# Optimization experiments

Measured on AMD Instinct MI355X. Metric: run time of the kernel, lower is better.

The kernel has to match this reference:

```python
import jax, jax.numpy as jnp
import numpy as np

B, L, D = 32, 2048, 128
SCALE = 1.0 / float(np.sqrt(D))  # scale = 1/sqrt(dim_K) per docstring


def setup_inputs() -> dict:
    key = jax.random.key(0)
    kq, kk, kv, kb = jax.random.split(key, 4)
    return {
        "Q": jax.random.normal(kq, (B, L, D), dtype=jnp.float32),
        "K": jax.random.normal(kk, (B, L, D), dtype=jnp.float32),
        "V": jax.random.normal(kv, (B, L, D), dtype=jnp.float32),
        "bias": jax.random.normal(kb, (L, L), dtype=jnp.float32),
    }


def reference(Q, K, V, bias):
    # scores = Q @ K^T + bias (bias broadcast over batch), then scale, softmax, @ V
    scores = jnp.einsum("bqd,bkd->bqk", Q, K) + bias[None, :, :]
    attn = jax.nn.softmax(scores * SCALE, axis=-1)  # [B, L, L]
    context = jnp.einsum("bqk,bkd->bqd", attn, V)   # [B, L, D]
    return (context, attn[0])
```

## Files before the change

### kernel.cpp

```cpp
#include <hip/hip_runtime.h>
#include <cstdint>
#include <cstddef>

#define L_ 2048
#define D_ 128
#define B_ 32
#define NT_ 32

static constexpr float SCALE = 0.08838834764831845f;
static constexpr float LOG2E = 1.4426950408889634f;
static constexpr float THR_  = 8.0f;

typedef __bf16 bf16x8 __attribute__((ext_vector_type(8)));
typedef __bf16 bf16x4 __attribute__((ext_vector_type(4)));
typedef float  f32x4  __attribute__((ext_vector_type(4)));
typedef int    i32x4  __attribute__((ext_vector_type(4)));

typedef const __attribute__((address_space(1))) uint32_t* gas_t;
typedef __attribute__((address_space(3))) uint32_t*       las_t;

__device__ __forceinline__ void dma16(const void* g, void* l) {
  __builtin_amdgcn_global_load_lds((gas_t)g, (las_t)l, 16, 0, 0);
}

__device__ __forceinline__ int cperm(int r) {
  return (r & 32) | (((r >> 3) & 1) << 4) | (((r >> 2) & 1) << 3)
       | (((r >> 4) & 1) << 2) | (r & 3);
}

__global__ __launch_bounds__(256) void prep_kv(
    const float* __restrict__ K, const float* __restrict__ V,
    __bf16* __restrict__ gK, __bf16* __restrict__ gVt)
{
  const int b   = blockIdx.x >> 5;
  const int kt  = blockIdx.x & 31;
  const int tid = threadIdx.x;
  const size_t tile = ((size_t)b * NT_ + kt) * 8192;

#pragma unroll
  for (int i = 0; i < 4; ++i) {
    const int g  = tid + i * 256;
    const int r  = g >> 4;
    const int c  = g & 15;
    const int d0 = (c ^ (r & 7)) * 8;
    const float* src = K + ((size_t)b * L_ + kt * 64 + r) * D_ + d0;
    float4 a = *(const float4*)src;
    float4 e = *(const float4*)(src + 4);
    bf16x8 f;
    f[0]=(__bf16)a.x; f[1]=(__bf16)a.y; f[2]=(__bf16)a.z; f[3]=(__bf16)a.w;
    f[4]=(__bf16)e.x; f[5]=(__bf16)e.y; f[6]=(__bf16)e.z; f[7]=(__bf16)e.w;
    *(bf16x8*)((char*)(gK + tile) + r * 256 + c * 16) = f;
  }

  __shared__ alignas(16) __bf16 Vt[8192];
  char* vb = (char*)Vt;
  const int vr     = tid & 63;
  const int vc     = cperm(vr);
  const int vdbase = (tid >> 6) * 32;
  const float* vrow = V + ((size_t)b * L_ + kt * 64 + vr) * D_ + vdbase;
#pragma unroll
  for (int c = 0; c < 8; ++c) {
    float4 v4 = *(const float4*)(vrow + c * 4);
    const int d0 = vdbase + c * 4;
    float vv[4] = {v4.x, v4.y, v4.z, v4.w};
#pragma unroll
    for (int jj = 0; jj < 4; ++jj) {
      const int d = d0 + jj;
      *(__bf16*)(vb + d * 128 + ((vc * 2) ^ ((d & 7) << 4))) = (__bf16)vv[jj];
    }
  }
  __syncthreads();
#pragma unroll
  for (int i = 0; i < 4; ++i) {
    const int off = (tid + i * 256) * 16;
    *(i32x4*)((char*)(gVt + tile) + off) = *(const i32x4*)(vb + off);
  }
}

__global__ __launch_bounds__(256) void prep_bias(
    const float* __restrict__ bias, float* __restrict__ biasS)
{
#pragma unroll
  for (int it = 0; it < 4; ++it) {
    const size_t idx = ((size_t)it * 1024 + blockIdx.x) * 256 + threadIdx.x;
    float4 v = ((const float4*)bias)[idx];
    v.x *= SCALE; v.y *= SCALE; v.z *= SCALE; v.w *= SCALE;
    ((float4*)biasS)[idx] = v;
  }
}

template<int MODE>
__global__ __launch_bounds__(256, 2) void attn_fwd(
    const float* __restrict__ Q, const float* __restrict__ K,
    const float* __restrict__ V, const float* __restrict__ bias,
    const float* __restrict__ biasS,
    const __bf16* __restrict__ gK, const __bf16* __restrict__ gVt,
    float* __restrict__ ctx, float* __restrict__ attn0)
{
  const int id   = blockIdx.x;
  const int idx  = id >> 3;
  const int b    = (id & 7) * 4 + (idx >> 4);
  const int qblk = idx & 15;

  const int tid  = threadIdx.x;
  const int wave = tid >> 6;
  const int lane = tid & 63;
  const int lg   = lane >> 4;
  const int lr   = lane & 15;

  const int qbase = qblk * 128 + wave * 32;

  constexpr int NBUF = (MODE >= 1) ? 2 : 1;
  __shared__ alignas(16) __bf16 Ksh[NBUF * 8192];
  __shared__ alignas(16) __bf16 Vtsh[NBUF * 8192];

  bf16x8 qf0[4], qf1[4];
#pragma unroll
  for (int h = 0; h < 2; ++h) {
    const float* qrow = Q + ((size_t)b * L_ + (qbase + h * 16 + lr)) * D_;
#pragma unroll
    for (int kc = 0; kc < 4; ++kc) {
      const int d0 = kc * 32 + lg * 8;
      float4 a = *(const float4*)(qrow + d0);
      float4 c = *(const float4*)(qrow + d0 + 4);
      bf16x8 f;
      f[0] = (__bf16)(a.x * SCALE); f[1] = (__bf16)(a.y * SCALE);
      f[2] = (__bf16)(a.z * SCALE); f[3] = (__bf16)(a.w * SCALE);
      f[4] = (__bf16)(c.x * SCALE); f[5] = (__bf16)(c.y * SCALE);
      f[6] = (__bf16)(c.z * SCALE); f[7] = (__bf16)(c.w * SCALE);
      if (h == 0) qf0[kc] = f; else qf1[kc] = f;
    }
  }

  f32x4 O0[8], O1[8];
#pragma unroll
  for (int i = 0; i < 8; ++i) {
    O0[i] = (f32x4){0.f, 0.f, 0.f, 0.f};
    O1[i] = (f32x4){0.f, 0.f, 0.f, 0.f};
  }
  float m0 = -3.0e38f, m1 = -3.0e38f;
  float lp0 = 0.f, lp1 = 0.f;

  auto stage_dma = [&](int kt, int bufsel) {
    const char* gk = (const char*)(gK + ((size_t)b * NT_ + kt) * 8192);
    const char* gv = (const char*)(gVt + ((size_t)b * NT_ + kt) * 8192);
    char* kdst = (char*)Ksh + bufsel * 16384;
    char* vdst = (char*)Vtsh + bufsel * 16384;
#pragma unroll
    for (int i = 0; i < 4; ++i) {
      const int off = (wave * 4 + i) * 1024;
      dma16(gk + off + lane * 16, kdst + off);
      dma16(gv + off + lane * 16, vdst + off);
    }
  };

  const float* bbase = (MODE == 2) ? biasS : bias;
  float4 bA[4], bB[4];
  auto load_bias = [&](int kvbase) {
    const float* p0 = bbase + (size_t)(qbase + lr) * L_ + kvbase + lg * 4;
    const float* p1 = p0 + (size_t)16 * L_;
#pragma unroll
    for (int t = 0; t < 4; ++t) {
      bA[t] = *(const float4*)(p0 + t * 16);
      bB[t] = *(const float4*)(p1 + t * 16);
    }
  };

  if constexpr (MODE >= 1) {
    stage_dma(0, 0);
    load_bias(0);
    stage_dma(1, 1);
  }

  for (int kt = 0; kt < NT_; ++kt) {
    const int kvbase = kt * 64;
    const int cur = (MODE >= 1) ? (kt & 1) : 0;
    const char* kb = (const char*)Ksh + cur * 16384;
    const char* vb = (const char*)Vtsh + cur * 16384;

    if constexpr (MODE >= 1) {
      if (kt < NT_ - 1) asm volatile("s_waitcnt vmcnt(16)" ::: "memory");
      else              asm volatile("s_waitcnt vmcnt(8)" ::: "memory");
      __builtin_amdgcn_s_barrier();
      __builtin_amdgcn_sched_barrier(0);
    } else {
#pragma unroll
      for (int it = 0; it < 8; ++it) {
        const int g  = tid + it * 256;
        const int r  = g >> 5;
        const int d0 = (g & 31) * 4;
        const size_t src = ((size_t)b * L_ + (kvbase + r)) * D_ + d0;
        float4 kv4 = *(const float4*)(K + src);
        bf16x4 k4 = {(__bf16)kv4.x, (__bf16)kv4.y, (__bf16)kv4.z, (__bf16)kv4.w};
        *(bf16x4*)((char*)Ksh + r * 256 + ((d0 * 2) ^ ((r & 7) << 4))) = k4;
      }
      {
        const int vr = tid & 63;
        const int vc = cperm(vr);
        const int vdbase = (tid >> 6) * 32;
        const float* vrow = V + ((size_t)b * L_ + (kvbase + vr)) * D_ + vdbase;
#pragma unroll
        for (int c = 0; c < 8; ++c) {
          float4 v4 = *(const float4*)(vrow + c * 4);
          const int d0 = vdbase + c * 4;
          float vv[4] = {v4.x, v4.y, v4.z, v4.w};
#pragma unroll
          for (int jj = 0; jj < 4; ++jj) {
            const int d = d0 + jj;
            *(__bf16*)((char*)Vtsh + d * 128 + ((vc * 2) ^ ((d & 7) << 4))) = (__bf16)vv[jj];
          }
        }
      }
      __syncthreads();
      load_bias(kvbase);
    }

    f32x4 S0[4], S1[4];
#pragma unroll
    for (int t = 0; t < 4; ++t) {
      S0[t] = (f32x4){0.f, 0.f, 0.f, 0.f};
      S1[t] = (f32x4){0.f, 0.f, 0.f, 0.f};
    }
    __builtin_amdgcn_s_setprio(1);
#pragma unroll
    for (int t = 0; t < 4; ++t) {
      const int r   = t * 16 + lr;
      const int swz = (r & 7) << 4;
#pragma unroll
      for (int kc = 0; kc < 4; ++kc) {
        const int d0 = kc * 32 + lg * 8;
        bf16x8 kf = *(const bf16x8*)(kb + r * 256 + ((d0 * 2) ^ swz));
        S0[t] = __builtin_amdgcn_mfma_f32_16x16x32_bf16(kf, qf0[kc], S0[t], 0, 0, 0);
        S1[t] = __builtin_amdgcn_mfma_f32_16x16x32_bf16(kf, qf1[kc], S1[t], 0, 0, 0);
      }
    }
    __builtin_amdgcn_s_setprio(0);

#pragma unroll
    for (int t = 0; t < 4; ++t) {
      if constexpr (MODE == 2) {
        S0[t][0] += bA[t].x; S0[t][1] += bA[t].y; S0[t][2] += bA[t].z; S0[t][3] += bA[t].w;
        S1[t][0] += bB[t].x; S1[t][1] += bB[t].y; S1[t][2] += bB[t].z; S1[t][3] += bB[t].w;
      } else {
        S0[t][0] = fmaf(bA[t].x, SCALE, S0[t][0]); S0[t][1] = fmaf(bA[t].y, SCALE, S0[t][1]);
        S0[t][2] = fmaf(bA[t].z, SCALE, S0[t][2]); S0[t][3] = fmaf(bA[t].w, SCALE, S0[t][3]);
        S1[t][0] = fmaf(bB[t].x, SCALE, S1[t][0]); S1[t][1] = fmaf(bB[t].y, SCALE, S1[t][1]);
        S1[t][2] = fmaf(bB[t].z, SCALE, S1[t][2]); S1[t][3] = fmaf(bB[t].w, SCALE, S1[t][3]);
      }
    }
    if (b == 0) {
      float* a0 = attn0 + (size_t)(qbase + lr) * L_ + kvbase + lg * 4;
      float* a1 = a0 + (size_t)16 * L_;
#pragma unroll
      for (int t = 0; t < 4; ++t) {
        *(float4*)(a0 + t * 16) = make_float4(S0[t][0], S0[t][1], S0[t][2], S0[t][3]);
        *(float4*)(a1 + t * 16) = make_float4(S1[t][0], S1[t][1], S1[t][2], S1[t][3]);
      }
    }

    float mt0 = fmaxf(fmaxf(fmaxf(S0[0][0], S0[0][1]), fmaxf(S0[0][2], S0[0][3])),
                      fmaxf(fmaxf(S0[1][0], S0[1][1]), fmaxf(S0[1][2], S0[1][3])));
    mt0 = fmaxf(mt0, fmaxf(fmaxf(S0[2][0], S0[2][1]), fmaxf(S0[2][2], S0[2][3])));
    mt0 = fmaxf(mt0, fmaxf(fmaxf(S0[3][0], S0[3][1]), fmaxf(S0[3][2], S0[3][3])));
    mt0 = fmaxf(mt0, __shfl_xor(mt0, 16));
    mt0 = fmaxf(mt0, __shfl_xor(mt0, 32));
    float mt1 = fmaxf(fmaxf(fmaxf(S1[0][0], S1[0][1]), fmaxf(S1[0][2], S1[0][3])),
                      fmaxf(fmaxf(S1[1][0], S1[1][1]), fmaxf(S1[1][2], S1[1][3])));
    mt1 = fmaxf(mt1, fmaxf(fmaxf(S1[2][0], S1[2][1]), fmaxf(S1[2][2], S1[2][3])));
    mt1 = fmaxf(mt1, fmaxf(fmaxf(S1[3][0], S1[3][1]), fmaxf(S1[3][2], S1[3][3])));
    mt1 = fmaxf(mt1, __shfl_xor(mt1, 16));
    mt1 = fmaxf(mt1, __shfl_xor(mt1, 32));

    if (__any((mt0 > m0 + THR_) || (mt1 > m1 + THR_))) {
      const float n0 = fmaxf(m0, mt0), c0 = exp2f((m0 - n0) * LOG2E);
      const float n1 = fmaxf(m1, mt1), c1 = exp2f((m1 - n1) * LOG2E);
      m0 = n0; m1 = n1; lp0 *= c0; lp1 *= c1;
      float cR0[4], cR1[4];
#pragma unroll
      for (int j = 0; j < 4; ++j) {
        cR0[j] = __shfl(c0, (lane & 0x30) | (lg * 4 + j));
        cR1[j] = __shfl(c1, (lane & 0x30) | (lg * 4 + j));
      }
#pragma unroll
      for (int dt = 0; dt < 8; ++dt) {
        O0[dt][0] *= cR0[0]; O0[dt][1] *= cR0[1]; O0[dt][2] *= cR0[2]; O0[dt][3] *= cR0[3];
        O1[dt][0] *= cR1[0]; O1[dt][1] *= cR1[1]; O1[dt][2] *= cR1[2]; O1[dt][3] *= cR1[3];
      }
    }

    bf16x4 pb0[4], pb1[4];
    const float mh0 = m0 * LOG2E, mh1 = m1 * LOG2E;
#pragma unroll
    for (int t = 0; t < 4; ++t) {
#pragma unroll
      for (int j = 0; j < 4; ++j) {
        const float p0 = exp2f(fmaf(S0[t][j], LOG2E, -mh0));
        const float p1 = exp2f(fmaf(S1[t][j], LOG2E, -mh1));
        lp0 += p0; lp1 += p1;
        pb0[t][j] = (__bf16)p0; pb1[t][j] = (__bf16)p1;
      }
    }

    __builtin_amdgcn_s_setprio(1);
#pragma unroll
    for (int kc2 = 0; kc2 < 2; ++kc2) {
      bf16x8 pa0, pa1;
      pa0[0] = pb0[kc2*2][0];   pa0[1] = pb0[kc2*2][1];
      pa0[2] = pb0[kc2*2][2];   pa0[3] = pb0[kc2*2][3];
      pa0[4] = pb0[kc2*2+1][0]; pa0[5] = pb0[kc2*2+1][1];
      pa0[6] = pb0[kc2*2+1][2]; pa0[7] = pb0[kc2*2+1][3];
      pa1[0] = pb1[kc2*2][0];   pa1[1] = pb1[kc2*2][1];
      pa1[2] = pb1[kc2*2][2];   pa1[3] = pb1[kc2*2][3];
      pa1[4] = pb1[kc2*2+1][0]; pa1[5] = pb1[kc2*2+1][1];
      pa1[6] = pb1[kc2*2+1][2]; pa1[7] = pb1[kc2*2+1][3];
      const int c0 = kc2 * 32;
#pragma unroll
      for (int dt = 0; dt < 8; ++dt) {
        const int d = dt * 16 + lr;
        bf16x8 vf = *(const bf16x8*)(vb + d * 128 + (((c0 + lg * 8) * 2) ^ ((d & 7) << 4)));
        O0[dt] = __builtin_amdgcn_mfma_f32_16x16x32_bf16(pa0, vf, O0[dt], 0, 0, 0);
        O1[dt] = __builtin_amdgcn_mfma_f32_16x16x32_bf16(pa1, vf, O1[dt], 0, 0, 0);
      }
    }
    __builtin_amdgcn_s_setprio(0);

    if constexpr (MODE >= 1) {
      __builtin_amdgcn_sched_barrier(0);
      __builtin_amdgcn_s_barrier();
      __builtin_amdgcn_sched_barrier(0);
      if (kt + 1 < NT_) load_bias((kt + 1) * 64);
      if (kt + 2 < NT_) stage_dma(kt + 2, cur);
    } else {
      __syncthreads();
    }
  }

  float ls0 = lp0;
  ls0 += __shfl_xor(ls0, 16);
  ls0 += __shfl_xor(ls0, 32);
  float ls1 = lp1;
  ls1 += __shfl_xor(ls1, 16);
  ls1 += __shfl_xor(ls1, 32);
  const float li0 = 1.f / ls0, li1 = 1.f / ls1;
  float iR0[4], iR1[4];
#pragma unroll
  for (int j = 0; j < 4; ++j) {
    iR0[j] = __shfl(li0, (lane & 0x30) | (lg * 4 + j));
    iR1[j] = __shfl(li1, (lane & 0x30) | (lg * 4 + j));
  }
#pragma unroll
  for (int dt = 0; dt < 8; ++dt) {
    const int d = dt * 16 + lr;
#pragma unroll
    for (int j = 0; j < 4; ++j) {
      const int q0 = qbase + lg * 4 + j;
      ctx[((size_t)b * L_ + q0) * D_ + d]      = O0[dt][j] * iR0[j];
      ctx[((size_t)b * L_ + q0 + 16) * D_ + d] = O1[dt][j] * iR1[j];
    }
  }
}

__global__ __launch_bounds__(256) void softmax_rows(float* __restrict__ attn0)
{
  const int row  = blockIdx.x;
  float* p = attn0 + (size_t)row * L_;
  const int tid  = threadIdx.x;
  const int wave = tid >> 6;
  const int lane = tid & 63;
  __shared__ float red[8];

  float4 a = ((const float4*)p)[tid];
  float4 c = ((const float4*)p)[tid + 256];
  float v[8] = {a.x, a.y, a.z, a.w, c.x, c.y, c.z, c.w};

  float mx = v[0];
#pragma unroll
  for (int i = 1; i < 8; ++i) mx = fmaxf(mx, v[i]);
#pragma unroll
  for (int msk = 1; msk < 64; msk <<= 1) mx = fmaxf(mx, __shfl_xor(mx, msk));
  if (lane == 0) red[wave] = mx;
  __syncthreads();
  mx = fmaxf(fmaxf(red[0], red[1]), fmaxf(red[2], red[3]));

  float e[8];
  float s = 0.f;
#pragma unroll
  for (int i = 0; i < 8; ++i) { e[i] = exp2f((v[i] - mx) * LOG2E); s += e[i]; }
#pragma unroll
  for (int msk = 1; msk < 64; msk <<= 1) s += __shfl_xor(s, msk);
  if (lane == 0) red[4 + wave] = s;
  __syncthreads();
  s = red[4] + red[5] + red[6] + red[7];
  const float inv = 1.f / s;

  float4 o0 = {e[0] * inv, e[1] * inv, e[2] * inv, e[3] * inv};
  float4 o1 = {e[4] * inv, e[5] * inv, e[6] * inv, e[7] * inv};
  ((float4*)p)[tid]       = o0;
  ((float4*)p)[tid + 256] = o1;
}

extern "C" void kernel_launch(void* const* d_in, const int* in_sizes, int n_in,
                              void* d_out, int out_size, void* d_ws, size_t ws_size,
                              hipStream_t stream) {
  const float* Q    = (const float*)d_in[0];
  const float* K    = (const float*)d_in[1];
  const float* V    = (const float*)d_in[2];
  const float* bias = (const float*)d_in[3];
  float* ctx   = (float*)d_out;
  float* attn0 = ctx + (size_t)B_ * L_ * D_;

  const size_t kvElems  = (size_t)B_ * L_ * D_;
  const size_t needKV   = 2 * kvElems * sizeof(__bf16);
  const size_t needAll  = needKV + (size_t)L_ * L_ * sizeof(float);

  __bf16* gK    = (__bf16*)d_ws;
  __bf16* gVt   = gK + kvElems;
  float*  biasS = (float*)(gVt + kvElems);

  if (ws_size >= needAll) {
    prep_kv<<<dim3(B_ * NT_), 256, 0, stream>>>(K, V, gK, gVt);
    prep_bias<<<dim3(1024), 256, 0, stream>>>(bias, biasS);
    attn_fwd<2><<<dim3(512), 256, 0, stream>>>(Q, K, V, bias, biasS, gK, gVt, ctx, attn0);
  } else if (ws_size >= needKV) {
    prep_kv<<<dim3(B_ * NT_), 256, 0, stream>>>(K, V, gK, gVt);
    attn_fwd<1><<<dim3(512), 256, 0, stream>>>(Q, K, V, bias, nullptr, gK, gVt, ctx, attn0);
  } else {
    attn_fwd<0><<<dim3(512), 256, 0, stream>>>(Q, K, V, bias, nullptr, nullptr, nullptr, ctx, attn0);
  }
  softmax_rows<<<L_, 256, 0, stream>>>(attn0);
}
```

Measured before the change: 169.2 us.

## Split KV range across two blocks with partial-output combine kernel

The attention kernel now splits the 32 KV tiles into two halves and launches twice as many blocks. Each block writes an unnormalised partial output and per-row (max, sum) to workspace, and a new combine kernel merges the halves. Double-buffered LDS staging is replaced with single-buffered staging plus full barriers, and occupancy is raised to 4 blocks per CU. The prescaled-bias kernel and the standalone row softmax are removed in favour of a normalisation kernel that reuses the stored statistics. The cost is extra workspace traffic for the fp32 partial outputs and an extra launch, plus lost overlap of loads with compute.

After: 555.4 us. 228% more time.

```diff
diff --git a/kernel.cpp b/kernel.cpp
--- a/kernel.cpp
+++ b/kernel.cpp
@@ -77,30 +77,26 @@
   }
 }
 
-__global__ __launch_bounds__(256) void prep_bias(
-    const float* __restrict__ bias, float* __restrict__ biasS)
-{
-#pragma unroll
-  for (int it = 0; it < 4; ++it) {
-    const size_t idx = ((size_t)it * 1024 + blockIdx.x) * 256 + threadIdx.x;
-    float4 v = ((const float4*)bias)[idx];
-    v.x *= SCALE; v.y *= SCALE; v.z *= SCALE; v.w *= SCALE;
-    ((float4*)biasS)[idx] = v;
-  }
-}
-
-template<int MODE>
-__global__ __launch_bounds__(256, 2) void attn_fwd(
+template<int SPLIT, int MODE>
+__global__ __launch_bounds__(256, 4) void attn_fwd(
     const float* __restrict__ Q, const float* __restrict__ K,
     const float* __restrict__ V, const float* __restrict__ bias,
-    const float* __restrict__ biasS,
     const __bf16* __restrict__ gK, const __bf16* __restrict__ gVt,
-    float* __restrict__ ctx, float* __restrict__ attn0)
+    float* __restrict__ ctx, float* __restrict__ attn0,
+    float* __restrict__ Opart, float2* __restrict__ ml)
 {
-  const int id   = blockIdx.x;
-  const int idx  = id >> 3;
-  const int b    = (id & 7) * 4 + (idx >> 4);
-  const int qblk = idx & 15;
+  const int id = blockIdx.x;
+  int half, b, qblk;
+  if constexpr (SPLIT) {
+    half = id >> 9;
+    const int rem = id & 511;
+    b    = rem >> 4;
+    qblk = rem & 15;
+  } else {
+    half = 0; b = id >> 4; qblk = id & 15;
+  }
+  const int kt0 = SPLIT ? half * (NT_ / 2) : 0;
+  const int ktN = SPLIT ? kt0 + (NT_ / 2) : NT_;
 
   const int tid  = threadIdx.x;
   const int wave = tid >> 6;
@@ -110,9 +106,10 @@
 
   const int qbase = qblk * 128 + wave * 32;
 
-  constexpr int NBUF = (MODE >= 1) ? 2 : 1;
-  __shared__ alignas(16) __bf16 Ksh[NBUF * 8192];
-  __shared__ alignas(16) __bf16 Vtsh[NBUF * 8192];
+  __shared__ alignas(16) __bf16 Ksh[8192];
+  __shared__ alignas(16) __bf16 Vtsh[8192];
+  const char* kb = (const char*)Ksh;
+  const char* vb = (const char*)Vtsh;
 
   bf16x8 qf0[4], qf1[4];
 #pragma unroll
@@ -141,23 +138,20 @@
   float m0 = -3.0e38f, m1 = -3.0e38f;
   float lp0 = 0.f, lp1 = 0.f;
 
-  auto stage_dma = [&](int kt, int bufsel) {
+  auto stage_dma = [&](int kt) {
     const char* gk = (const char*)(gK + ((size_t)b * NT_ + kt) * 8192);
     const char* gv = (const char*)(gVt + ((size_t)b * NT_ + kt) * 8192);
-    char* kdst = (char*)Ksh + bufsel * 16384;
-    char* vdst = (char*)Vtsh + bufsel * 16384;
 #pragma unroll
     for (int i = 0; i < 4; ++i) {
       const int off = (wave * 4 + i) * 1024;
-      dma16(gk + off + lane * 16, kdst + off);
-      dma16(gv + off + lane * 16, vdst + off);
+      dma16(gk + off + lane * 16, (char*)Ksh + off);
+      dma16(gv + off + lane * 16, (char*)Vtsh + off);
     }
   };
 
-  const float* bbase = (MODE == 2) ? biasS : bias;
   float4 bA[4], bB[4];
   auto load_bias = [&](int kvbase) {
-    const float* p0 = bbase + (size_t)(qbase + lr) * L_ + kvbase + lg * 4;
+    const float* p0 = bias + (size_t)(qbase + lr) * L_ + kvbase + lg * 4;
     const float* p1 = p0 + (size_t)16 * L_;
 #pragma unroll
     for (int t = 0; t < 4; ++t) {
@@ -166,24 +160,12 @@
     }
   };
 
-  if constexpr (MODE >= 1) {
-    stage_dma(0, 0);
-    load_bias(0);
-    stage_dma(1, 1);
-  }
-
-  for (int kt = 0; kt < NT_; ++kt) {
+  if constexpr (MODE >= 1) { stage_dma(kt0); load_bias(kt0 * 64); }
+
+  for (int kt = kt0; kt < ktN; ++kt) {
     const int kvbase = kt * 64;
-    const int cur = (MODE >= 1) ? (kt & 1) : 0;
-    const char* kb = (const char*)Ksh + cur * 16384;
-    const char* vb = (const char*)Vtsh + cur * 16384;
-
-    if constexpr (MODE >= 1) {
-      if (kt < NT_ - 1) asm volatile("s_waitcnt vmcnt(16)" ::: "memory");
-      else              asm volatile("s_waitcnt vmcnt(8)" ::: "memory");
-      __builtin_amdgcn_s_barrier();
-      __builtin_amdgcn_sched_barrier(0);
-    } else {
+
+    if constexpr (MODE == 0) {
 #pragma unroll
       for (int it = 0; it < 8; ++it) {
         const int g  = tid + it * 256;
@@ -211,9 +193,9 @@
           }
         }
       }
-      __syncthreads();
-      load_bias(kvbase);
-    }
+    }
+    __syncthreads();
+    if constexpr (MODE == 0) load_bias(kvbase);
 
     f32x4 S0[4], S1[4];
 #pragma unroll
@@ -238,15 +220,10 @@
 
 #pragma unroll
     for (int t = 0; t < 4; ++t) {
-      if constexpr (MODE == 2) {
-        S0[t][0] += bA[t].x; S0[t][1] += bA[t].y; S0[t][2] += bA[t].z; S0[t][3] += bA[t].w;
-        S1[t][0] += bB[t].x; S1[t][1] += bB[t].y; S1[t][2] += bB[t].z; S1[t][3] += bB[t].w;
-      } else {
-        S0[t][0] = fmaf(bA[t].x, SCALE, S0[t][0]); S0[t][1] = fmaf(bA[t].y, SCALE, S0[t][1]);
-        S0[t][2] = fmaf(bA[t].z, SCALE, S0[t][2]); S0[t][3] = fmaf(bA[t].w, SCALE, S0[t][3]);
-        S1[t][0] = fmaf(bB[t].x, SCALE, S1[t][0]); S1[t][1] = fmaf(bB[t].y, SCALE, S1[t][1]);
-        S1[t][2] = fmaf(bB[t].z, SCALE, S1[t][2]); S1[t][3] = fmaf(bB[t].w, SCALE, S1[t][3]);
-      }
+      S0[t][0] = fmaf(bA[t].x, SCALE, S0[t][0]); S0[t][1] = fmaf(bA[t].y, SCALE, S0[t][1]);
+      S0[t][2] = fmaf(bA[t].z, SCALE, S0[t][2]); S0[t][3] = fmaf(bA[t].w, SCALE, S0[t][3]);
+      S1[t][0] = fmaf(bB[t].x, SCALE, S1[t][0]); S1[t][1] = fmaf(bB[t].y, SCALE, S1[t][1]);
+      S1[t][2] = fmaf(bB[t].z, SCALE, S1[t][2]); S1[t][3] = fmaf(bB[t].w, SCALE, S1[t][3]);
     }
     if (b == 0) {
       float* a0 = attn0 + (size_t)(qbase + lr) * L_ + kvbase + lg * 4;
@@ -324,79 +301,111 @@
     }
     __builtin_amdgcn_s_setprio(0);
 
+    __syncthreads();
     if constexpr (MODE >= 1) {
-      __builtin_amdgcn_sched_barrier(0);
-      __builtin_amdgcn_s_barrier();
-      __builtin_amdgcn_sched_barrier(0);
-      if (kt + 1 < NT_) load_bias((kt + 1) * 64);
-      if (kt + 2 < NT_) stage_dma(kt + 2, cur);
-    } else {
-      __syncthreads();
-    }
-  }
-
-  float ls0 = lp0;
-  ls0 += __shfl_xor(ls0, 16);
-  ls0 += __shfl_xor(ls0, 32);
-  float ls1 = lp1;
-  ls1 += __shfl_xor(ls1, 16);
-  ls1 += __shfl_xor(ls1, 32);
-  const float li0 = 1.f / ls0, li1 = 1.f / ls1;
-  float iR0[4], iR1[4];
-#pragma unroll
-  for (int j = 0; j < 4; ++j) {
-    iR0[j] = __shfl(li0, (lane & 0x30) | (lg * 4 + j));
-    iR1[j] = __shfl(li1, (lane & 0x30) | (lg * 4 + j));
-  }
-#pragma unroll
-  for (int dt = 0; dt < 8; ++dt) {
-    const int d = dt * 16 + lr;
+      if (kt + 1 < ktN) { load_bias((kt + 1) * 64); stage_dma(kt + 1); }
+    }
+  }
+
+  float ls0 = lp0; ls0 += __shfl_xor(ls0, 16); ls0 += __shfl_xor(ls0, 32);
+  float ls1 = lp1; ls1 += __shfl_xor(ls1, 16); ls1 += __shfl_xor(ls1, 32);
+
+  if constexpr (SPLIT) {
+    float* Obase = Opart + ((size_t)half * B_ + b) * L_ * D_;
+#pragma unroll
+    for (int dt = 0; dt < 8; ++dt) {
+      const int d = dt * 16 + lr;
+#pragma unroll
+      for (int j = 0; j < 4; ++j) {
+        const int q0 = qbase + lg * 4 + j;
+        Obase[(size_t)q0 * D_ + d]        = O0[dt][j];
+        Obase[(size_t)(q0 + 16) * D_ + d] = O1[dt][j];
+      }
+    }
+    if (lg == 0) {
+      float2* mlb = ml + ((size_t)half * B_ + b) * L_;
+      mlb[qbase + lr]      = make_float2(m0, ls0);
+      mlb[qbase + 16 + lr] = make_float2(m1, ls1);
+    }
+  } else {
+    const float li0 = 1.f / ls0, li1 = 1.f / ls1;
+    float iR0[4], iR1[4];
 #pragma unroll
     for (int j = 0; j < 4; ++j) {
-      const int q0 = qbase + lg * 4 + j;
-      ctx[((size_t)b * L_ + q0) * D_ + d]      = O0[dt][j] * iR0[j];
-      ctx[((size_t)b * L_ + q0 + 16) * D_ + d] = O1[dt][j] * iR1[j];
-    }
-  }
-}
-
-__global__ __launch_bounds__(256) void softmax_rows(float* __restrict__ attn0)
+      iR0[j] = __shfl(li0, (lane & 0x30) | (lg * 4 + j));
+      iR1[j] = __shfl(li1, (lane & 0x30) | (lg * 4 + j));
+    }
+#pragma unroll
+    for (int dt = 0; dt < 8; ++dt) {
+      const int d = dt * 16 + lr;
+#pragma unroll
+      for (int j = 0; j < 4; ++j) {
+        const int q0 = qbase + lg * 4 + j;
+        ctx[((size_t)b * L_ + q0) * D_ + d]        = O0[dt][j] * iR0[j];
+        ctx[((size_t)b * L_ + q0 + 16) * D_ + d]   = O1[dt][j] * iR1[j];
+      }
+    }
+    if (b == 0) {
+#pragma unroll 1
+      for (int rr = 0; rr < 32; ++rr) {
+        const float mr = __shfl(rr < 16 ? m0 : m1, rr & 15) * LOG2E;
+        const float iv = __shfl(rr < 16 ? li0 : li1, rr & 15);
+        float4* rowp = (float4*)(attn0 + (size_t)(qbase + rr) * L_);
+#pragma unroll
+        for (int c = 0; c < 8; ++c) {
+          float4 v = rowp[c * 64 + lane];
+          v.x = exp2f(fmaf(v.x, LOG2E, -mr)) * iv;
+          v.y = exp2f(fmaf(v.y, LOG2E, -mr)) * iv;
+          v.z = exp2f(fmaf(v.z, LOG2E, -mr)) * iv;
+          v.w = exp2f(fmaf(v.w, LOG2E, -mr)) * iv;
+          rowp[c * 64 + lane] = v;
+        }
+      }
+    }
+  }
+}
+
+__global__ __launch_bounds__(256) void combine(
+    const float* __restrict__ Opart, const float2* __restrict__ ml,
+    float* __restrict__ ctx)
 {
-  const int row  = blockIdx.x;
-  float* p = attn0 + (size_t)row * L_;
-  const int tid  = threadIdx.x;
-  const int wave = tid >> 6;
-  const int lane = tid & 63;
-  __shared__ float red[8];
-
-  float4 a = ((const float4*)p)[tid];
-  float4 c = ((const float4*)p)[tid + 256];
-  float v[8] = {a.x, a.y, a.z, a.w, c.x, c.y, c.z, c.w};
-
-  float mx = v[0];
-#pragma unroll
-  for (int i = 1; i < 8; ++i) mx = fmaxf(mx, v[i]);
-#pragma unroll
-  for (int msk = 1; msk < 64; msk <<= 1) mx = fmaxf(mx, __shfl_xor(mx, msk));
-  if (lane == 0) red[wave] = mx;
-  __syncthreads();
-  mx = fmaxf(fmaxf(red[0], red[1]), fmaxf(red[2], red[3]));
-
-  float e[8];
-  float s = 0.f;
-#pragma unroll
-  for (int i = 0; i < 8; ++i) { e[i] = exp2f((v[i] - mx) * LOG2E); s += e[i]; }
-#pragma unroll
-  for (int msk = 1; msk < 64; msk <<= 1) s += __shfl_xor(s, msk);
-  if (lane == 0) red[4 + wave] = s;
-  __syncthreads();
-  s = red[4] + red[5] + red[6] + red[7];
-  const float inv = 1.f / s;
-
-  float4 o0 = {e[0] * inv, e[1] * inv, e[2] * inv, e[3] * inv};
-  float4 o1 = {e[4] * inv, e[5] * inv, e[6] * inv, e[7] * inv};
-  ((float4*)p)[tid]       = o0;
-  ((float4*)p)[tid + 256] = o1;
+  const int r = blockIdx.x * 8 + (threadIdx.x >> 5);
+  const int c = threadIdx.x & 31;
+  const float2 a = ml[r];
+  const float2 e = ml[(size_t)B_ * L_ + r];
+  const float m  = fmaxf(a.x, e.x);
+  float w0 = exp2f((a.x - m) * LOG2E);
+  float w1 = exp2f((e.x - m) * LOG2E);
+  const float inv = 1.f / (a.y * w0 + e.y * w1);
+  w0 *= inv; w1 *= inv;
+  const float4 x = ((const float4*)Opart)[(size_t)r * 32 + c];
+  const float4 y = ((const float4*)(Opart + (size_t)B_ * L_ * D_))[(size_t)r * 32 + c];
+  float4 o = {x.x * w0 + y.x * w1, x.y * w0 + y.y * w1,
+              x.z * w0 + y.z * w1, x.w * w0 + y.w * w1};
+  ((float4*)ctx)[(size_t)r * 32 + c] = o;
+}
+
+__global__ __launch_bounds__(256) void attn0_norm(
+    float* __restrict__ attn0, const float2* __restrict__ ml)
+{
+  const int row = blockIdx.x;
+  const float2 a = ml[row];
+  const float2 e = ml[(size_t)B_ * L_ + row];
+  const float m  = fmaxf(a.x, e.x);
+  const float l  = a.y * exp2f((a.x - m) * LOG2E) + e.y * exp2f((e.x - m) * LOG2E);
+  const float inv = 1.f / l;
+  const float mh  = m * LOG2E;
+  float4* p = (float4*)(attn0 + (size_t)row * L_);
+#pragma unroll
+  for (int i = 0; i < 2; ++i) {
+    const int idx = threadIdx.x + i * 256;
+    float4 v = p[idx];
+    v.x = exp2f(fmaf(v.x, LOG2E, -mh)) * inv;
+    v.y = exp2f(fmaf(v.y, LOG2E, -mh)) * inv;
+    v.z = exp2f(fmaf(v.z, LOG2E, -mh)) * inv;
+    v.w = exp2f(fmaf(v.w, LOG2E, -mh)) * inv;
+    p[idx] = v;
+  }
 }
 
 extern "C" void kernel_launch(void* const* d_in, const int* in_sizes, int n_in,
@@ -410,22 +419,27 @@
   float* attn0 = ctx + (size_t)B_ * L_ * D_;
 
   const size_t kvElems  = (size_t)B_ * L_ * D_;
-  const size_t needKV   = 2 * kvElems * sizeof(__bf16);
-  const size_t needAll  = needKV + (size_t)L_ * L_ * sizeof(float);
+  const size_t imgBytes = 2 * kvElems * sizeof(__bf16);
+  const size_t opBytes  = 2 * kvElems * sizeof(float);
+  const size_t mlBytes  = (size_t)2 * B_ * L_ * sizeof(float2);
 
   __bf16* gK    = (__bf16*)d_ws;
   __bf16* gVt   = gK + kvElems;
-  float*  biasS = (float*)(gVt + kvElems);
-
-  if (ws_size >= needAll) {
+  float*  Opart = (float*)(gVt + kvElems);
+  float2* ml    = (float2*)(Opart + 2 * kvElems);
+
+  if (ws_size >= imgBytes + opBytes + mlBytes) {
     prep_kv<<<dim3(B_ * NT_), 256, 0, stream>>>(K, V, gK, gVt);
-    prep_bias<<<dim3(1024), 256, 0, stream>>>(bias, biasS);
-    attn_fwd<2><<<dim3(512), 256, 0, stream>>>(Q, K, V, bias, biasS, gK, gVt, ctx, attn0);
-  } else if (ws_size >= needKV) {
+    attn_fwd<1, 1><<<dim3(1024), 256, 0, stream>>>(Q, K, V, bias, gK, gVt,
+                                                   ctx, attn0, Opart, ml);
+    combine<<<dim3(B_ * L_ / 8), 256, 0, stream>>>(Opart, ml, ctx);
+    attn0_norm<<<dim3(L_), 256, 0, stream>>>(attn0, ml);
+  } else if (ws_size >= imgBytes) {
     prep_kv<<<dim3(B_ * NT_), 256, 0, stream>>>(K, V, gK, gVt);
-    attn_fwd<1><<<dim3(512), 256, 0, stream>>>(Q, K, V, bias, nullptr, gK, gVt, ctx, attn0);
+    attn_fwd<0, 1><<<dim3(512), 256, 0, stream>>>(Q, K, V, bias, gK, gVt,
+                                                  ctx, attn0, nullptr, nullptr);
   } else {
-    attn_fwd<0><<<dim3(512), 256, 0, stream>>>(Q, K, V, bias, nullptr, nullptr, nullptr, ctx, attn0);
-  }
-  softmax_rows<<<L_, 256, 0, stream>>>(attn0);
-}
+    attn_fwd<0, 0><<<dim3(512), 256, 0, stream>>>(Q, K, V, bias, nullptr, nullptr,
+                                                  ctx, attn0, nullptr, nullptr);
+  }
+}
```
